# Kernel tuning notes

Hardware: AMD Instinct MI355X
Metric: run time of the kernel (lower is better)

Reference implementation:

```python
import jax, jax.numpy as jnp
import numpy as np

EPS = 1e-6
INPUT_SIZE = 64
NUM_LEAVES = INPUT_SIZE
NUM_LAYERS = NUM_LEAVES - 1
BATCH = 262144
SINKHORN_ITERS = 20


def _clip01(v):
    return jnp.clip(v, EPS, 1.0 - EPS)


def _F_base(x, y, a, w0, w1):
    # Branches of F for a in [0.5, 2] (the non-recursive region), selected branchlessly.
    x = _clip01(x)
    y = _clip01(y)
    lin = w0 * x + w1 * y
    p = jnp.sqrt(3.0 / jnp.maximum(2.0 - a, EPS)) - 1.0
    g = (x ** (2.0 * w0) * y ** (2.0 * w1)) ** p
    rule0 = jnp.where((jnp.abs(x - 1.0) < EPS) & (jnp.abs(y - 1.0) < EPS), 1.0, 0.0)
    return jnp.where(
        jnp.abs(a - 2.0) < EPS, rule0,
        jnp.where(a >= 0.75, g,
                  jnp.where(a > 0.5, (3.0 - 4.0 * a) * lin + (4.0 * a - 2.0) * g, lin)))


def _F(x, y, a, w0, w1):
    # Full generalized_gcd F with the single-level De Morgan reflection for a < 0.5.
    x = _clip01(x)
    y = _clip01(y)
    hi = _F_base(x, y, a, w0, w1)
    a_ref = jnp.clip(1.0 - a, -1.0 + EPS, 2.0 - EPS)
    lo = 1.0 - _F_base(1.0 - x, 1.0 - y, a_ref, w0, w1)
    lin = w0 * x + w1 * y
    return jnp.where(jnp.abs(a - 0.5) < EPS, lin, jnp.where(a < 0.5, lo, hi))


def _sinkhorn(logits, n_iter=SINKHORN_ITERS):
    # Log-space Sinkhorn normalization -> (approximately) doubly-stochastic P.
    l = logits
    for _ in range(n_iter):
        l = l - jax.nn.logsumexp(l, axis=1, keepdims=True)
        l = l - jax.nn.logsumexp(l, axis=0, keepdims=True)
    return jnp.exp(l)


def setup_inputs() -> dict:
    key = jax.random.key(0)
    k1, k2, k3, k4 = jax.random.split(key, 4)
    x = jax.random.uniform(k1, (BATCH, INPUT_SIZE), dtype=jnp.float32)
    logits = jax.random.normal(k2, (INPUT_SIZE, NUM_LEAVES), dtype=jnp.float32)
    weights = jax.random.uniform(k3, (NUM_LAYERS,), dtype=jnp.float32)
    biases = jax.random.uniform(k4, (NUM_LAYERS,), dtype=jnp.float32)
    return {"x": x, "logits": logits, "weights": weights, "biases": biases}


def reference(x, logits, weights, biases):
    P = _sinkhorn(logits)                 # [INPUT_SIZE, NUM_LEAVES], columns sum to 1
    leaves = (x @ P).T                    # [NUM_LEAVES, BATCH]

    def step(carry, inp):
        leaf, w, b = inp
        nres = _F(carry, leaf, b, w, 1.0 - w)
        nres = jnp.where(jnp.isnan(nres), b, nres)  # NaN fallback to bias, as in torch forward
        return nres, None

    # Left-leaning tree: state_0 = leaf_0; state_i = F(state_{i-1}, leaf_i, b, w, 1-w)
    final, _ = jax.lax.scan(step, leaves[0], (leaves[1:], weights, biases))
    return final[:, None]                 # [BATCH, 1]
```

## Files before the change

### kernel.cpp

```cpp
#include <hip/hip_runtime.h>
#include <hip/hip_bf16.h>
#include <math.h>

#define EPS 1e-6f
#define N 64
#define NLAYERS 63
#define SINK_ITERS 20
#define LOG2E 1.4426950408889634f

typedef __attribute__((ext_vector_type(8))) short bf16x8;
typedef __attribute__((ext_vector_type(4))) float f32x4;

__device__ __forceinline__ float fast_log2(float v) {
#if __has_builtin(__builtin_amdgcn_logf)
  return __builtin_amdgcn_logf(v);
#else
  return log2f(v);
#endif
}
__device__ __forceinline__ float fast_exp2(float v) {
#if __has_builtin(__builtin_amdgcn_exp2f)
  return __builtin_amdgcn_exp2f(v);
#else
  return exp2f(v);
#endif
}

__device__ __forceinline__ unsigned short f2bf(float f) {
  unsigned int u = __float_as_uint(f);
  return (unsigned short)((u + 0x7FFFu + ((u >> 16) & 1u)) >> 16);
}

__device__ __forceinline__ unsigned int cvt_pk_bf16(float lo, float hi) {
  unsigned int r;
  asm("v_cvt_pk_bf16_f32 %0, %1, %2" : "=v"(r) : "v"(lo), "v"(hi));
  return r;
}
__device__ __forceinline__ bf16x8 pack8(float4 a, float4 b) {
  union { unsigned int ui[4]; bf16x8 v; } u;
  u.ui[0] = cvt_pk_bf16(a.x, a.y);
  u.ui[1] = cvt_pk_bf16(a.z, a.w);
  u.ui[2] = cvt_pk_bf16(b.x, b.y);
  u.ui[3] = cvt_pk_bf16(b.z, b.w);
  return u.v;
}

__global__ __launch_bounds__(64) void sinkhorn_kernel(
    const float* __restrict__ logits,
    const float* __restrict__ weights,
    const float* __restrict__ biases,
    unsigned short* __restrict__ Pfrag,
    float* __restrict__ layers) {
  __shared__ float T[64 * 65 + 128];
  const int l = threadIdx.x;

  float K[64];
  {
    const float4* lr = (const float4*)(logits + (l << 6));
    #pragma unroll
    for (int q = 0; q < 16; ++q) {
      float4 t = lr[q];
      K[4*q+0] = fast_exp2(t.x * LOG2E);
      K[4*q+1] = fast_exp2(t.y * LOG2E);
      K[4*q+2] = fast_exp2(t.z * LOG2E);
      K[4*q+3] = fast_exp2(t.w * LOG2E);
    }
  }
  #pragma unroll
  for (int j = 0; j < 64; ++j) T[l * 65 + j] = K[j];
  __syncthreads();
  float KT[64];
  #pragma unroll
  for (int k = 0; k < 64; ++k) KT[k] = T[k * 65 + l];
  __syncthreads();

  float* Uv = &T[64 * 65];
  float* Vv = &T[64 * 65 + 64];
  const float4* Uv4 = (const float4*)Uv;
  const float4* Vv4 = (const float4*)Vv;
  Vv[l] = 1.0f;
  __syncthreads();

  float u = 1.0f;
  for (int it = 0; it < SINK_ITERS; ++it) {
    float s0 = 0.f, s1 = 0.f, s2 = 0.f, s3 = 0.f;
    #pragma unroll
    for (int q = 0; q < 16; ++q) {
      float4 v = Vv4[q];
      s0 = fmaf(K[4*q+0], v.x, s0);
      s1 = fmaf(K[4*q+1], v.y, s1);
      s2 = fmaf(K[4*q+2], v.z, s2);
      s3 = fmaf(K[4*q+3], v.w, s3);
    }
    u = 1.0f / ((s0 + s1) + (s2 + s3));
    __syncthreads();
    Uv[l] = u;
    __syncthreads();
    float c0 = 0.f, c1 = 0.f, c2 = 0.f, c3 = 0.f;
    #pragma unroll
    for (int q = 0; q < 16; ++q) {
      float4 uu = Uv4[q];
      c0 = fmaf(KT[4*q+0], uu.x, c0);
      c1 = fmaf(KT[4*q+1], uu.y, c1);
      c2 = fmaf(KT[4*q+2], uu.z, c2);
      c3 = fmaf(KT[4*q+3], uu.w, c3);
    }
    float v = 1.0f / ((c0 + c1) + (c2 + c3));
    __syncthreads();
    Vv[l] = v;
    __syncthreads();
  }

  #pragma unroll
  for (int j = 0; j < 64; ++j) T[l * 65 + j] = u * K[j] * Vv[j];
  __syncthreads();

  #pragma unroll
  for (int s = 0; s < 2; ++s)
    #pragma unroll
    for (int t = 0; t < 4; ++t) {
      union { unsigned short us[8]; bf16x8 v; } buf;
      #pragma unroll
      for (int j = 0; j < 8; ++j)
        buf.us[j] = f2bf(T[(s*32 + ((l >> 4) << 3) + j) * 65 + t*16 + (l & 15)]);
      *(bf16x8*)(Pfrag + (((s*4 + t) * 64 + l) << 3)) = buf.v;
    }

  if (l < NLAYERS) {
    float w0 = weights[l];
    float w1 = 1.0f - w0;
    float a  = biases[l];
    float sgn, e0, e1, cw0, cw1, lcg;
    if (fabsf(a - 0.5f) < EPS) {
      sgn = 1.f; e0 = 0.f; e1 = 0.f; cw0 = w0; cw1 = w1; lcg = -1.0e30f;
    } else {
      float ae;
      if (a < 0.5f) { sgn = -1.f; ae = fminf(fmaxf(1.0f - a, -1.0f + EPS), 2.0f - EPS); }
      else          { sgn =  1.f; ae = a; }
      float pp = sqrtf(3.0f / fmaxf(2.0f - ae, EPS)) - 1.0f;
      float cl, cg;
      if (ae >= 0.75f) { cl = 0.0f;            cg = 1.0f; }
      else             { cl = 3.0f - 4.0f*ae;  cg = 4.0f*ae - 2.0f; }
      e0  = 2.0f * w0 * pp;
      e1  = 2.0f * w1 * pp;
      cw0 = cl * w0;
      cw1 = cl * w1;
      lcg = (cg > 0.f) ? log2f(cg) : -1.0e30f;
    }
    float sgnp = 1.f;
    if (l > 0) {
      float ap = biases[l - 1];
      sgnp = (fabsf(ap - 0.5f) < EPS) ? 1.f : (ap < 0.5f ? -1.f : 1.f);
    }
    float Sc = sgn * sgnp;
    float Oc = 0.5f - 0.5f * Sc;
    float* Lr = layers + l * 8;
    Lr[0] = sgn; Lr[1] = e1; Lr[2] = lcg; Lr[3] = cw1;
    Lr[4] = Sc;  Lr[5] = Oc; Lr[6] = e0;  Lr[7] = cw0;
  }
}


template<int HALF>
__device__ __forceinline__ void do_gemm(const bf16x8 (&Bf)[2][4],
                                        const bf16x8 (&Af)[4][2],
                                        float* Lv, int w, int q, int c) {
  #pragma unroll
  for (int rt = 0; rt < 4; ++rt) {
    #pragma unroll
    for (int lt = 0; lt < 2; ++lt) {
      f32x4 acc = {0.f, 0.f, 0.f, 0.f};
      acc = __builtin_amdgcn_mfma_f32_16x16x32_bf16(Bf[0][(HALF << 1) + lt], Af[rt][0], acc, 0, 0, 0);
      acc = __builtin_amdgcn_mfma_f32_16x16x32_bf16(Bf[1][(HALF << 1) + lt], Af[rt][1], acc, 0, 0, 0);
      const int row  = (w << 6) + (rt << 4) + c;
      const int nloc = (lt << 4) + (q << 2);
      *(f32x4*)&Lv[row * 36 + nloc] = acc;
    }
  }
}

__device__ __forceinline__ void do_chunk(int L0, const float* Lrow,
                                         const float4* Lp4, float& r) {
  const int loc = L0 & 31;
  f32x4 lf0 = *(const f32x4*)&Lrow[loc];
  f32x4 lf1 = *(const f32x4*)&Lrow[loc + 4];
  float lf[8] = {lf0[0], lf0[1], lf0[2], lf0[3], lf1[0], lf1[1], lf1[2], lf1[3]};

  float ylin[8], ylg[8];
  #pragma unroll
  for (int k = 0; k < 8; ++k) {
    if (L0 + k >= 1) {
      float4 p0 = Lp4[(L0 + k - 1) * 2];
      float off = fmaf(-0.5f, p0.x, 0.5f);
      float yy  = fminf(fmaxf(lf[k], EPS), 1.0f - EPS);
      float yr  = fmaf(p0.x, yy, off);
      float ly  = fast_log2(yr);
      ylg[k]  = fmaf(p0.y, ly, p0.z);
      ylin[k] = p0.w * yr;
    }
  }

  #pragma unroll
  for (int k = 0; k < 8; ++k) {
    if (L0 + k >= 1) {
      float4 p1 = Lp4[(L0 + k - 1) * 2 + 1];
      float cr = fminf(fmaxf(r, EPS), 1.0f - EPS);
      float xr = fmaf(p1.x, cr, p1.y);
      float lx = fast_log2(xr);
      float g  = fast_exp2(fmaf(p1.z, lx, ylg[k]));
      r = fmaf(p1.w, xr, ylin[k]) + g;
    } else {
      r = lf[0];
    }
  }
}

__global__ __launch_bounds__(256, 4) void scan_kernel(
    const float* __restrict__ x,
    const unsigned short* __restrict__ Pfrag,
    const float* __restrict__ layers,
    float* __restrict__ out) {
  __shared__ float Lv[256 * 36];
  const int tid = threadIdx.x;
  const int w = tid >> 6, l = tid & 63;
  const int q = l >> 4, c = l & 15;
  const size_t rowbase = (size_t)blockIdx.x << 8;
  const float4* Lp4 = (const float4*)layers;

  float4 xa[4][4];
  #pragma unroll
  for (int i = 0; i < 4; ++i) {
    const float* rp = x + (rowbase + (w << 6) + (i << 4) + c) * 64 + (q << 3);
    xa[i][0] = *(const float4*)(rp);
    xa[i][1] = *(const float4*)(rp + 4);
    xa[i][2] = *(const float4*)(rp + 32);
    xa[i][3] = *(const float4*)(rp + 36);
  }

  bf16x8 Bf[2][4];
  #pragma unroll
  for (int s = 0; s < 2; ++s)
    #pragma unroll
    for (int t = 0; t < 4; ++t)
      Bf[s][t] = *(const bf16x8*)(Pfrag + (((s*4 + t) * 64 + l) << 3));

  bf16x8 Af[4][2];
  #pragma unroll
  for (int i = 0; i < 4; ++i) {
    Af[i][0] = pack8(xa[i][0], xa[i][1]);
    Af[i][1] = pack8(xa[i][2], xa[i][3]);
  }

  float r = 0.f;
  const float* Lrow = &Lv[tid * 36];

  do_gemm<0>(Bf, Af, Lv, w, q, c);
  #pragma unroll 1
  for (int cch = 0; cch < 4; ++cch)
    do_chunk(cch * 8, Lrow, Lp4, r);

  do_gemm<1>(Bf, Af, Lv, w, q, c);
  #pragma unroll 1
  for (int cch = 0; cch < 4; ++cch)
    do_chunk(32 + cch * 8, Lrow, Lp4, r);

  const float sgnL = layers[62 * 8];
  out[rowbase + tid] = fmaf(sgnL, r, fmaf(-0.5f, sgnL, 0.5f));
}

extern "C" void kernel_launch(void* const* d_in, const int* in_sizes, int n_in,
                              void* d_out, int out_size, void* d_ws, size_t ws_size,
                              hipStream_t stream) {
  const float* x       = (const float*)d_in[0];
  const float* logits  = (const float*)d_in[1];
  const float* weights = (const float*)d_in[2];
  const float* biases  = (const float*)d_in[3];
  float* out = (float*)d_out;

  unsigned short* Pfrag = (unsigned short*)d_ws;
  float* layers = (float*)((char*)d_ws + 8 * 64 * 8 * sizeof(unsigned short));

  const int batch = out_size;

  hipLaunchKernelGGL(sinkhorn_kernel, dim3(1), dim3(64), 0, stream,
                     logits, weights, biases, Pfrag, layers);
  hipLaunchKernelGGL(scan_kernel, dim3(batch / 256), dim3(256), 0, stream,
                     x, Pfrag, layers, out);
}
```

Measured before the change: 119.8 us.

## Fuse Sinkhorn prologue into scan kernel, recomputing per block over two row tiles

Drops the separate single-block Sinkhorn launch. Every block of the scan kernel now recomputes the Sinkhorn matrix and per-layer constants in its first wave, synchronising only within that wave, and keeps them in shared memory. Each block now handles 512 rows in two passes to spread the redundant prologue, and the chunk loop is fully unrolled with compile-time offsets. The aim is to remove the serial tiny-kernel latency and the global round trip, at the cost of redundant compute per block, more shared memory and lower occupancy (launch bounds 2).

```diff
diff --git a/kernel.cpp b/kernel.cpp
--- a/kernel.cpp
+++ b/kernel.cpp
@@ -3,7 +3,6 @@
 #include <math.h>
 
 #define EPS 1e-6f
-#define N 64
 #define NLAYERS 63
 #define SINK_ITERS 20
 #define LOG2E 1.4426950408889634f
@@ -45,120 +44,7 @@
   return u.v;
 }
 
-__global__ __launch_bounds__(64) void sinkhorn_kernel(
-    const float* __restrict__ logits,
-    const float* __restrict__ weights,
-    const float* __restrict__ biases,
-    unsigned short* __restrict__ Pfrag,
-    float* __restrict__ layers) {
-  __shared__ float T[64 * 65 + 128];
-  const int l = threadIdx.x;
-
-  float K[64];
-  {
-    const float4* lr = (const float4*)(logits + (l << 6));
-    #pragma unroll
-    for (int q = 0; q < 16; ++q) {
-      float4 t = lr[q];
-      K[4*q+0] = fast_exp2(t.x * LOG2E);
-      K[4*q+1] = fast_exp2(t.y * LOG2E);
-      K[4*q+2] = fast_exp2(t.z * LOG2E);
-      K[4*q+3] = fast_exp2(t.w * LOG2E);
-    }
-  }
-  #pragma unroll
-  for (int j = 0; j < 64; ++j) T[l * 65 + j] = K[j];
-  __syncthreads();
-  float KT[64];
-  #pragma unroll
-  for (int k = 0; k < 64; ++k) KT[k] = T[k * 65 + l];
-  __syncthreads();
-
-  float* Uv = &T[64 * 65];
-  float* Vv = &T[64 * 65 + 64];
-  const float4* Uv4 = (const float4*)Uv;
-  const float4* Vv4 = (const float4*)Vv;
-  Vv[l] = 1.0f;
-  __syncthreads();
-
-  float u = 1.0f;
-  for (int it = 0; it < SINK_ITERS; ++it) {
-    float s0 = 0.f, s1 = 0.f, s2 = 0.f, s3 = 0.f;
-    #pragma unroll
-    for (int q = 0; q < 16; ++q) {
-      float4 v = Vv4[q];
-      s0 = fmaf(K[4*q+0], v.x, s0);
-      s1 = fmaf(K[4*q+1], v.y, s1);
-      s2 = fmaf(K[4*q+2], v.z, s2);
-      s3 = fmaf(K[4*q+3], v.w, s3);
-    }
-    u = 1.0f / ((s0 + s1) + (s2 + s3));
-    __syncthreads();
-    Uv[l] = u;
-    __syncthreads();
-    float c0 = 0.f, c1 = 0.f, c2 = 0.f, c3 = 0.f;
-    #pragma unroll
-    for (int q = 0; q < 16; ++q) {
-      float4 uu = Uv4[q];
-      c0 = fmaf(KT[4*q+0], uu.x, c0);
-      c1 = fmaf(KT[4*q+1], uu.y, c1);
-      c2 = fmaf(KT[4*q+2], uu.z, c2);
-      c3 = fmaf(KT[4*q+3], uu.w, c3);
-    }
-    float v = 1.0f / ((c0 + c1) + (c2 + c3));
-    __syncthreads();
-    Vv[l] = v;
-    __syncthreads();
-  }
-
-  #pragma unroll
-  for (int j = 0; j < 64; ++j) T[l * 65 + j] = u * K[j] * Vv[j];
-  __syncthreads();
-
-  #pragma unroll
-  for (int s = 0; s < 2; ++s)
-    #pragma unroll
-    for (int t = 0; t < 4; ++t) {
-      union { unsigned short us[8]; bf16x8 v; } buf;
-      #pragma unroll
-      for (int j = 0; j < 8; ++j)
-        buf.us[j] = f2bf(T[(s*32 + ((l >> 4) << 3) + j) * 65 + t*16 + (l & 15)]);
-      *(bf16x8*)(Pfrag + (((s*4 + t) * 64 + l) << 3)) = buf.v;
-    }
-
-  if (l < NLAYERS) {
-    float w0 = weights[l];
-    float w1 = 1.0f - w0;
-    float a  = biases[l];
-    float sgn, e0, e1, cw0, cw1, lcg;
-    if (fabsf(a - 0.5f) < EPS) {
-      sgn = 1.f; e0 = 0.f; e1 = 0.f; cw0 = w0; cw1 = w1; lcg = -1.0e30f;
-    } else {
-      float ae;
-      if (a < 0.5f) { sgn = -1.f; ae = fminf(fmaxf(1.0f - a, -1.0f + EPS), 2.0f - EPS); }
-      else          { sgn =  1.f; ae = a; }
-      float pp = sqrtf(3.0f / fmaxf(2.0f - ae, EPS)) - 1.0f;
-      float cl, cg;
-      if (ae >= 0.75f) { cl = 0.0f;            cg = 1.0f; }
-      else             { cl = 3.0f - 4.0f*ae;  cg = 4.0f*ae - 2.0f; }
-      e0  = 2.0f * w0 * pp;
-      e1  = 2.0f * w1 * pp;
-      cw0 = cl * w0;
-      cw1 = cl * w1;
-      lcg = (cg > 0.f) ? log2f(cg) : -1.0e30f;
-    }
-    float sgnp = 1.f;
-    if (l > 0) {
-      float ap = biases[l - 1];
-      sgnp = (fabsf(ap - 0.5f) < EPS) ? 1.f : (ap < 0.5f ? -1.f : 1.f);
-    }
-    float Sc = sgn * sgnp;
-    float Oc = 0.5f - 0.5f * Sc;
-    float* Lr = layers + l * 8;
-    Lr[0] = sgn; Lr[1] = e1; Lr[2] = lcg; Lr[3] = cw1;
-    Lr[4] = Sc;  Lr[5] = Oc; Lr[6] = e0;  Lr[7] = cw0;
-  }
-}
+__device__ __forceinline__ void wave_fence() { asm volatile("" ::: "memory"); }
 
 
 template<int HALF>
@@ -179,9 +65,10 @@
   }
 }
 
-__device__ __forceinline__ void do_chunk(int L0, const float* Lrow,
-                                         const float4* Lp4, float& r) {
-  const int loc = L0 & 31;
+template<int L0>
+__device__ __forceinline__ void do_chunk(const float* Lrow,
+                                         const float* Lcst, float& r) {
+  constexpr int loc = L0 & 31;
   f32x4 lf0 = *(const f32x4*)&Lrow[loc];
   f32x4 lf1 = *(const f32x4*)&Lrow[loc + 4];
   float lf[8] = {lf0[0], lf0[1], lf0[2], lf0[3], lf1[0], lf1[1], lf1[2], lf1[3]};
@@ -190,7 +77,7 @@
   #pragma unroll
   for (int k = 0; k < 8; ++k) {
     if (L0 + k >= 1) {
-      float4 p0 = Lp4[(L0 + k - 1) * 2];
+      float4 p0 = *(const float4*)&Lcst[(L0 + k - 1) * 8];
       float off = fmaf(-0.5f, p0.x, 0.5f);
       float yy  = fminf(fmaxf(lf[k], EPS), 1.0f - EPS);
       float yr  = fmaf(p0.x, yy, off);
@@ -203,7 +90,7 @@
   #pragma unroll
   for (int k = 0; k < 8; ++k) {
     if (L0 + k >= 1) {
-      float4 p1 = Lp4[(L0 + k - 1) * 2 + 1];
+      float4 p1 = *(const float4*)&Lcst[(L0 + k - 1) * 8 + 4];
       float cr = fminf(fmaxf(r, EPS), 1.0f - EPS);
       float xr = fmaf(p1.x, cr, p1.y);
       float lx = fast_log2(xr);
@@ -215,35 +102,55 @@
   }
 }
 
-__global__ __launch_bounds__(256, 4) void scan_kernel(
+__device__ __forceinline__ void run_pass(const bf16x8 (&Bf)[2][4],
+                                         const bf16x8 (&Af)[4][2],
+                                         float* Lv, const float* Lcst,
+                                         float* __restrict__ out,
+                                         size_t rowbase, int tid,
+                                         int w, int q, int c) {
+  const float* Lrow = &Lv[tid * 36];
+  float r = 0.f;
+
+  do_gemm<0>(Bf, Af, Lv, w, q, c);
+  do_chunk<0>(Lrow, Lcst, r);
+  do_chunk<8>(Lrow, Lcst, r);
+  do_chunk<16>(Lrow, Lcst, r);
+  do_chunk<24>(Lrow, Lcst, r);
+
+  do_gemm<1>(Bf, Af, Lv, w, q, c);
+  do_chunk<32>(Lrow, Lcst, r);
+  do_chunk<40>(Lrow, Lcst, r);
+  do_chunk<48>(Lrow, Lcst, r);
+  do_chunk<56>(Lrow, Lcst, r);
+
+  const float sgnL = Lcst[62 * 8];
+  out[rowbase + tid] = fmaf(sgnL, r, fmaf(-0.5f, sgnL, 0.5f));
+}
+
+__global__ __launch_bounds__(256, 2) void fused_kernel(
     const float* __restrict__ x,
-    const unsigned short* __restrict__ Pfrag,
-    const float* __restrict__ layers,
+    const float* __restrict__ logits,
+    const float* __restrict__ weights,
+    const float* __restrict__ biases,
     float* __restrict__ out) {
+  __shared__ float T[64 * 65 + 128];
+  __shared__ float Lcst[NLAYERS * 8];
   __shared__ float Lv[256 * 36];
+
   const int tid = threadIdx.x;
   const int w = tid >> 6, l = tid & 63;
   const int q = l >> 4, c = l & 15;
-  const size_t rowbase = (size_t)blockIdx.x << 8;
-  const float4* Lp4 = (const float4*)layers;
+  const size_t rowbase0 = (size_t)blockIdx.x << 9;
 
   float4 xa[4][4];
   #pragma unroll
   for (int i = 0; i < 4; ++i) {
-    const float* rp = x + (rowbase + (w << 6) + (i << 4) + c) * 64 + (q << 3);
+    const float* rp = x + (rowbase0 + (w << 6) + (i << 4) + c) * 64 + (q << 3);
     xa[i][0] = *(const float4*)(rp);
     xa[i][1] = *(const float4*)(rp + 4);
     xa[i][2] = *(const float4*)(rp + 32);
     xa[i][3] = *(const float4*)(rp + 36);
   }
-
-  bf16x8 Bf[2][4];
-  #pragma unroll
-  for (int s = 0; s < 2; ++s)
-    #pragma unroll
-    for (int t = 0; t < 4; ++t)
-      Bf[s][t] = *(const bf16x8*)(Pfrag + (((s*4 + t) * 64 + l) << 3));
-
   bf16x8 Af[4][2];
   #pragma unroll
   for (int i = 0; i < 4; ++i) {
@@ -251,21 +158,132 @@
     Af[i][1] = pack8(xa[i][2], xa[i][3]);
   }
 
-  float r = 0.f;
-  const float* Lrow = &Lv[tid * 36];
-
-  do_gemm<0>(Bf, Af, Lv, w, q, c);
-  #pragma unroll 1
-  for (int cch = 0; cch < 4; ++cch)
-    do_chunk(cch * 8, Lrow, Lp4, r);
-
-  do_gemm<1>(Bf, Af, Lv, w, q, c);
-  #pragma unroll 1
-  for (int cch = 0; cch < 4; ++cch)
-    do_chunk(32 + cch * 8, Lrow, Lp4, r);
-
-  const float sgnL = layers[62 * 8];
-  out[rowbase + tid] = fmaf(sgnL, r, fmaf(-0.5f, sgnL, 0.5f));
+  if (tid < 64) {
+    float K[64];
+    {
+      const float4* lr = (const float4*)(logits + (l << 6));
+      #pragma unroll
+      for (int p = 0; p < 16; ++p) {
+        float4 t = lr[p];
+        K[4*p+0] = fast_exp2(t.x * LOG2E);
+        K[4*p+1] = fast_exp2(t.y * LOG2E);
+        K[4*p+2] = fast_exp2(t.z * LOG2E);
+        K[4*p+3] = fast_exp2(t.w * LOG2E);
+      }
+    }
+    #pragma unroll
+    for (int j = 0; j < 64; ++j) T[l * 65 + j] = K[j];
+    wave_fence();
+    float KT[64];
+    #pragma unroll
+    for (int k = 0; k < 64; ++k) KT[k] = T[k * 65 + l];
+    wave_fence();
+
+    float* Uv = &T[64 * 65];
+    float* Vv = &T[64 * 65 + 64];
+    const float4* Uv4 = (const float4*)Uv;
+    const float4* Vv4 = (const float4*)Vv;
+    Vv[l] = 1.0f;
+    wave_fence();
+
+    float u = 1.0f;
+    for (int it = 0; it < SINK_ITERS; ++it) {
+      float s0 = 0.f, s1 = 0.f, s2 = 0.f, s3 = 0.f;
+      #pragma unroll
+      for (int p = 0; p < 16; ++p) {
+        float4 v = Vv4[p];
+        s0 = fmaf(K[4*p+0], v.x, s0);
+        s1 = fmaf(K[4*p+1], v.y, s1);
+        s2 = fmaf(K[4*p+2], v.z, s2);
+        s3 = fmaf(K[4*p+3], v.w, s3);
+      }
+      u = 1.0f / ((s0 + s1) + (s2 + s3));
+      Uv[l] = u;
+      wave_fence();
+      float c0 = 0.f, c1 = 0.f, c2 = 0.f, c3 = 0.f;
+      #pragma unroll
+      for (int p = 0; p < 16; ++p) {
+        float4 uu = Uv4[p];
+        c0 = fmaf(KT[4*p+0], uu.x, c0);
+        c1 = fmaf(KT[4*p+1], uu.y, c1);
+        c2 = fmaf(KT[4*p+2], uu.z, c2);
+        c3 = fmaf(KT[4*p+3], uu.w, c3);
+      }
+      float v = 1.0f / ((c0 + c1) + (c2 + c3));
+      Vv[l] = v;
+      wave_fence();
+    }
+
+    #pragma unroll
+    for (int j = 0; j < 64; ++j) T[l * 65 + j] = u * K[j] * Vv[j];
+
+    if (l < NLAYERS) {
+      float w0 = weights[l];
+      float w1 = 1.0f - w0;
+      float a  = biases[l];
+      float sgn, e0, e1, cw0, cw1, lcg;
+      if (fabsf(a - 0.5f) < EPS) {
+        sgn = 1.f; e0 = 0.f; e1 = 0.f; cw0 = w0; cw1 = w1; lcg = -1.0e30f;
+      } else {
+        float ae;
+        if (a < 0.5f) { sgn = -1.f; ae = fminf(fmaxf(1.0f - a, -1.0f + EPS), 2.0f - EPS); }
+        else          { sgn =  1.f; ae = a; }
+        float pp = sqrtf(3.0f / fmaxf(2.0f - ae, EPS)) - 1.0f;
+        float cl, cg;
+        if (ae >= 0.75f) { cl = 0.0f;            cg = 1.0f; }
+        else             { cl = 3.0f - 4.0f*ae;  cg = 4.0f*ae - 2.0f; }
+        e0  = 2.0f * w0 * pp;
+        e1  = 2.0f * w1 * pp;
+        cw0 = cl * w0;
+        cw1 = cl * w1;
+        lcg = (cg > 0.f) ? log2f(cg) : -1.0e30f;
+      }
+      float sgnp = 1.f;
+      if (l > 0) {
+        float ap = biases[l - 1];
+        sgnp = (fabsf(ap - 0.5f) < EPS) ? 1.f : (ap < 0.5f ? -1.f : 1.f);
+      }
+      float Sc = sgn * sgnp;
+      float Oc = 0.5f - 0.5f * Sc;
+      float* Lr = Lcst + l * 8;
+      Lr[0] = sgn; Lr[1] = e1; Lr[2] = lcg; Lr[3] = cw1;
+      Lr[4] = Sc;  Lr[5] = Oc; Lr[6] = e0;  Lr[7] = cw0;
+    }
+  }
+  __syncthreads();
+
+  bf16x8 Bf[2][4];
+  #pragma unroll
+  for (int s = 0; s < 2; ++s)
+    #pragma unroll
+    for (int t = 0; t < 4; ++t) {
+      union { unsigned short us[8]; bf16x8 v; } buf;
+      #pragma unroll
+      for (int j = 0; j < 8; ++j)
+        buf.us[j] = f2bf(T[(s*32 + (q << 3) + j) * 65 + t*16 + c]);
+      Bf[s][t] = buf.v;
+    }
+
+  run_pass(Bf, Af, Lv, Lcst, out, rowbase0, tid, w, q, c);
+
+  {
+    float4 xb[4][4];
+    #pragma unroll
+    for (int i = 0; i < 4; ++i) {
+      const float* rp = x + (rowbase0 + 256 + (w << 6) + (i << 4) + c) * 64 + (q << 3);
+      xb[i][0] = *(const float4*)(rp);
+      xb[i][1] = *(const float4*)(rp + 4);
+      xb[i][2] = *(const float4*)(rp + 32);
+      xb[i][3] = *(const float4*)(rp + 36);
+    }
+    bf16x8 Af2[4][2];
+    #pragma unroll
+    for (int i = 0; i < 4; ++i) {
+      Af2[i][0] = pack8(xb[i][0], xb[i][1]);
+      Af2[i][1] = pack8(xb[i][2], xb[i][3]);
+    }
+    run_pass(Bf, Af2, Lv, Lcst, out, rowbase0 + 256, tid, w, q, c);
+  }
 }
 
 extern "C" void kernel_launch(void* const* d_in, const int* in_sizes, int n_in,
@@ -277,13 +295,7 @@
   const float* biases  = (const float*)d_in[3];
   float* out = (float*)d_out;
 
-  unsigned short* Pfrag = (unsigned short*)d_ws;
-  float* layers = (float*)((char*)d_ws + 8 * 64 * 8 * sizeof(unsigned short));
-
   const int batch = out_size;
-
-  hipLaunchKernelGGL(sinkhorn_kernel, dim3(1), dim3(64), 0, stream,
-                     logits, weights, biases, Pfrag, layers);
-  hipLaunchKernelGGL(scan_kernel, dim3(batch / 256), dim3(256), 0, stream,
-                     x, Pfrag, layers, out);
-}
+  hipLaunchKernelGGL(fused_kernel, dim3(batch / 512), dim3(256), 0, stream,
+                     x, logits, weights, biases, out);
+}
```

Result: slower. 190.8 us (+59.2%).
